# Optimization experiments

Hardware: AMD Instinct MI355X
Metric: run time of the kernel (lower is better)

Reference implementation:

```python
import jax, jax.numpy as jnp
import numpy as np

B, DIM, L, H, W = 4, 128, 256, 8, 8
N = L * H * W
D_INNER, D_STATE, D_CONV, DT_RANK = 128, 8, 4, 8


def _ln(x, w, b, eps=1e-5):
    m = x.mean(-1, keepdims=True)
    v = ((x - m) ** 2).mean(-1, keepdims=True)
    return (x - m) * jax.lax.rsqrt(v + eps) * w + b


def _mamba_fusion(x, z_in, p, i):
    # x, z_in: (B, N, DIM). x drives the SSM; z_in provides the cross-modal gate.
    u = x @ p['Wx'][i]                                    # (B, N, D_INNER)
    z = z_in @ p['Wz'][i]                                 # (B, N, D_INNER)
    # causal depthwise conv1d along tokens, kernel D_CONV (torch pad=k-1 then truncate)
    up = jnp.pad(u, ((0, 0), (D_CONV - 1, 0), (0, 0)))
    w = p['conv_w'][i]                                    # (D_INNER, D_CONV)
    uc = sum(up[:, k:k + u.shape[1], :] * w[:, k] for k in range(D_CONV)) + p['conv_b'][i]
    uc = jax.nn.silu(uc)
    x_dbl = uc @ p['Wxproj'][i]                           # (B, N, DT_RANK + 2*D_STATE)
    dt_r, Bm, Cm = jnp.split(x_dbl, [DT_RANK, DT_RANK + D_STATE], axis=-1)
    dt = jax.nn.softplus(dt_r @ p['Wdt'][i] + p['bdt'][i])  # (B, N, D_INNER)
    A = -jnp.exp(p['A_log'][i])                           # (D_INNER, D_STATE)
    dA = jnp.exp(dt[..., None] * A)                       # (B, N, D_INNER, D_STATE)
    dBu = dt[..., None] * Bm[:, :, None, :] * uc[..., None]

    def step(h, inp):
        dA_t, dBu_t, C_t = inp
        h = dA_t * h + dBu_t                              # (B, D_INNER, D_STATE)
        return h, jnp.einsum('bds,bs->bd', h, C_t)

    h0 = jnp.zeros((u.shape[0], D_INNER, D_STATE), u.dtype)
    _, ys = jax.lax.scan(step, h0, (dA.swapaxes(0, 1), dBu.swapaxes(0, 1), Cm.swapaxes(0, 1)))
    y = ys.swapaxes(0, 1) + p['Dp'][i] * uc
    y = y * jax.nn.silu(z)
    return y @ p['Wout_m'][i] + p['bout_m'][i]


def _cross_block(in0, in1, p, i):
    skip = in0
    a = _ln(in0, p['ln0_w'][i], p['ln0_b'][i])
    b = _ln(in1, p['ln1_w'][i], p['ln1_b'][i])
    return skip + _mamba_fusion(a, b, p, i)


def setup_inputs() -> dict:
    key = jax.random.key(0)
    ks = jax.random.split(key, 16)
    s_in = 1.0 / np.sqrt(DIM)
    s_di = 1.0 / np.sqrt(D_INNER)
    inp = {
        'front': jax.random.normal(ks[0], (B, DIM, L, H, W), jnp.float32),
        'back': jax.random.normal(ks[1], (B, DIM, L, H, W), jnp.float32),
        'ln0_w': jnp.ones((2, DIM), jnp.float32),
        'ln0_b': jnp.zeros((2, DIM), jnp.float32),
        'ln1_w': jnp.ones((2, DIM), jnp.float32),
        'ln1_b': jnp.zeros((2, DIM), jnp.float32),
        'Wx': jax.random.normal(ks[2], (2, DIM, D_INNER), jnp.float32) * s_in,
        'Wz': jax.random.normal(ks[3], (2, DIM, D_INNER), jnp.float32) * s_in,
        'conv_w': jax.random.normal(ks[4], (2, D_INNER, D_CONV), jnp.float32) * 0.5,
        'conv_b': jnp.zeros((2, D_INNER), jnp.float32),
        'Wxproj': jax.random.normal(ks[5], (2, D_INNER, DT_RANK + 2 * D_STATE), jnp.float32) * s_di,
        'Wdt': jax.random.normal(ks[6], (2, DT_RANK, D_INNER), jnp.float32) * (1.0 / np.sqrt(DT_RANK)),
        'bdt': jnp.full((2, D_INNER), -4.6, jnp.float32),  # softplus^-1(~0.01)
        'A_log': jnp.broadcast_to(jnp.log(jnp.arange(1, D_STATE + 1, dtype=jnp.float32)), (2, D_INNER, D_STATE)).copy(),
        'Dp': jnp.ones((2, D_INNER), jnp.float32),
        'Wout_m': jax.random.normal(ks[7], (2, D_INNER, DIM), jnp.float32) * s_di,
        'bout_m': jnp.zeros((2, DIM), jnp.float32),
        'Wout': jax.random.normal(ks[8], (DIM, DIM), jnp.float32) * s_in,
        'bout': jnp.zeros((DIM,), jnp.float32),
    }
    return inp


def reference(front, back, ln0_w, ln0_b, ln1_w, ln1_b, Wx, Wz, conv_w, conv_b,
              Wxproj, Wdt, bdt, A_log, Dp, Wout_m, bout_m, Wout, bout):
    p = dict(ln0_w=ln0_w, ln0_b=ln0_b, ln1_w=ln1_w, ln1_b=ln1_b, Wx=Wx, Wz=Wz,
             conv_w=conv_w, conv_b=conv_b, Wxproj=Wxproj, Wdt=Wdt, bdt=bdt,
             A_log=A_log, Dp=Dp, Wout_m=Wout_m, bout_m=bout_m)
    ff = front.reshape(B, DIM, N).swapaxes(1, 2)          # (B, N, DIM)
    bf = back.reshape(B, DIM, N).swapaxes(1, 2)
    f_fus = _cross_block(ff, bf, p, 0)
    b_fus = _cross_block(bf, ff, p, 1)
    fusion = ((f_fus + b_fus) * 0.5) @ Wout + bout
    return fusion.swapaxes(1, 2).reshape(B, DIM, L, H, W)
```

## Files before the change

kernel.cpp:

```cpp
#include <hip/hip_runtime.h>

#define DEV static __device__ __forceinline__

typedef short s16x8 __attribute__((ext_vector_type(8)));
typedef float f32x4 __attribute__((ext_vector_type(4)));
typedef unsigned short u16;

DEV float b2f(u16 u){ return __uint_as_float(((unsigned int)u) << 16); }
DEV u16 f2b(float f){
  unsigned int x = __float_as_uint(f);
  x += 0x7fffu + ((x >> 16) & 1u);
  return (u16)(x >> 16);
}
DEV float silu_f(float x){ return x * __builtin_amdgcn_rcpf(1.f + __expf(-x)); }
DEV float softplus_f(float x){ return (x > 15.f) ? x : __logf(1.f + __expf(x)); }
DEV bool detf32(const void* lnw){ return *(const unsigned int*)lnw == 0x3F800000u; }
DEV float ldin(const void* p, long long i, bool f){
  return f ? ((const float*)p)[i] : b2f(((const u16*)p)[i]);
}

static constexpr int BATCH = 4;
static constexpr int NSEQ  = 16384;
static constexpr int RTOT  = BATCH * NSEQ;
static constexpr int GCH   = 256;
static constexpr int DIRSZ = BATCH*GCH*128*8;

__global__ __launch_bounds__(256) void k_setup(
                        const void* ln0w, const void* ln0b, const void* ln1w, const void* ln1b,
                        const void* Wx, const void* Wz, const void* Wxp, const void* Wdt,
                        const void* bdt, const void* Alog, const void* convw, const void* convb,
                        const void* Dpr, const void* Woutm, const void* boutm,
                        const void* Wout, const void* bout,
                        u16* Wuz, u16* WdtBC, u16* Wcat, u16* WoutT,
                        float* buz, float* bdtf, float* bcat, float* boutf,
                        float* Aexp, float* convwF, float* convbF, float* DpF)
{
  bool f = detf32(ln0w);
  int tid = blockIdx.x * 256 + threadIdx.x;
  int gs  = gridDim.x * 256;
  for (int idx = tid; idx < 2*256*128; idx += gs){
    int d = idx >> 15; int n = (idx >> 7) & 255; int k = idx & 127;
    float wv;
    if (n < 128) wv = ldin(ln0w, d*128+k, f) * ldin(Wx, (long long)(d*128+k)*128 + n, f);
    else         wv = ldin(ln1w, (1-d)*128+k, f) * ldin(Wz, (long long)((1-d)*128+k)*128 + (n-128), f);
    Wuz[idx] = f2b(wv);
  }
  for (int idx = tid; idx < 2*256; idx += gs){
    int d = idx >> 8; int n = idx & 255;
    float s = 0.f;
    if (n < 128){
      for (int k = 0; k < 128; ++k)
        s += ldin(ln0b, d*128+k, f) * ldin(Wx, (long long)(d*128+k)*128 + n, f);
    } else {
      for (int k = 0; k < 128; ++k)
        s += ldin(ln1b, (1-d)*128+k, f) * ldin(Wz, (long long)((1-d)*128+k)*128 + (n-128), f);
    }
    buz[idx] = s;
  }
  for (int idx = tid; idx < 2*128; idx += gs)
    bdtf[idx] = ldin(bdt, idx, f);
  for (int idx = tid; idx < 2*144*128; idx += gs){
    int i = idx / (144*128); int rem = idx % (144*128); int n = rem >> 7; int k = rem & 127;
    if (n < 128){
      float s = 0.f;
      for (int j = 0; j < 8; ++j)
        s += ldin(Wxp, (long long)(i*128+k)*24 + j, f) * ldin(Wdt, (long long)(i*8+j)*128 + n, f);
      WdtBC[idx] = f2b(s);
    } else {
      WdtBC[idx] = f2b(ldin(Wxp, (long long)(i*128+k)*24 + (n - 120), f));
    }
  }
  for (int idx = tid; idx < 128*256; idx += gs){
    int n = idx >> 8; int k = idx & 255;
    Wcat[idx] = f2b(ldin(Woutm, (long long)k*128 + n, f));
  }
  for (int idx = tid; idx < 128*128; idx += gs){
    int n = idx >> 7, k = idx & 127;
    WoutT[idx] = f2b(ldin(Wout, (long long)k*128 + n, f));
  }
  for (int idx = tid; idx < 128; idx += gs){
    bcat[idx]  = ldin(boutm, idx, f) + ldin(boutm, 128 + idx, f);
    boutf[idx] = ldin(bout, idx, f);
  }
  for (int idx = tid; idx < 2*128*8; idx += gs)
    Aexp[idx] = -expf(ldin(Alog, idx, f));
  for (int idx = tid; idx < 2*128*4; idx += gs)
    convwF[idx] = ldin(convw, idx, f);
  for (int idx = tid; idx < 2*128; idx += gs){
    convbF[idx] = ldin(convb, idx, f);
    DpF[idx]   = ldin(Dpr, idx, f);
  }
}

__global__ __launch_bounds__(256) void k_ln(const void* front, const void* back, const void* ln0w,
                                            u16* xf, u16* xb, u16* sfbh)
{
  bool fF = detf32(ln0w);
  __shared__ u16 Af[64][130];
  __shared__ u16 Ab[64][130];
  __shared__ float Mf[64], Rf[64], Mb[64], Rb[64];
  int tid = threadIdx.x;
  long long r0 = (long long)blockIdx.x * 64;
  int b  = (int)(r0 >> 14);
  int n0 = (int)(r0 & 16383);
  if (fF){
    const float* fp = (const float*)front;
    const float* bp = (const float*)back;
    for (int it = 0; it < 8; ++it){
      int d = it*16 + (tid >> 4);
      int t = (tid & 15) * 4;
      long long gi = ((long long)(b*128 + d))*NSEQ + n0 + t;
      float4 vf = *(const float4*)&fp[gi];
      float4 vb = *(const float4*)&bp[gi];
      Af[t+0][d] = f2b(vf.x); Af[t+1][d] = f2b(vf.y);
      Af[t+2][d] = f2b(vf.z); Af[t+3][d] = f2b(vf.w);
      Ab[t+0][d] = f2b(vb.x); Ab[t+1][d] = f2b(vb.y);
      Ab[t+2][d] = f2b(vb.z); Ab[t+3][d] = f2b(vb.w);
    }
  } else {
    const u16* fp = (const u16*)front;
    const u16* bp = (const u16*)back;
    for (int it = 0; it < 4; ++it){
      int d = it*32 + (tid >> 3);
      int t = (tid & 7) * 8;
      long long gi = ((long long)(b*128 + d))*NSEQ + n0 + t;
      uint4 vf = *(const uint4*)&fp[gi];
      uint4 vb = *(const uint4*)&bp[gi];
      Af[t+0][d] = (u16)vf.x; Af[t+1][d] = (u16)(vf.x>>16);
      Af[t+2][d] = (u16)vf.y; Af[t+3][d] = (u16)(vf.y>>16);
      Af[t+4][d] = (u16)vf.z; Af[t+5][d] = (u16)(vf.z>>16);
      Af[t+6][d] = (u16)vf.w; Af[t+7][d] = (u16)(vf.w>>16);
      Ab[t+0][d] = (u16)vb.x; Ab[t+1][d] = (u16)(vb.x>>16);
      Ab[t+2][d] = (u16)vb.y; Ab[t+3][d] = (u16)(vb.y>>16);
      Ab[t+4][d] = (u16)vb.z; Ab[t+5][d] = (u16)(vb.z>>16);
      Ab[t+6][d] = (u16)vb.w; Ab[t+7][d] = (u16)(vb.w>>16);
    }
  }
  __syncthreads();
  {
    int t = tid >> 2, sub = tid & 3;
    float s = 0.f, ss = 0.f, s2 = 0.f, ss2 = 0.f;
    for (int k = 0; k < 32; ++k){
      float v = b2f(Af[t][sub*32 + k]); s  += v; ss  += v*v;
      float w = b2f(Ab[t][sub*32 + k]); s2 += w; ss2 += w*w;
    }
    for (int m = 1; m < 4; m <<= 1){
      s  += __shfl_xor(s,  m, 64); ss  += __shfl_xor(ss,  m, 64);
      s2 += __shfl_xor(s2, m, 64); ss2 += __shfl_xor(ss2, m, 64);
    }
    if (sub == 0){
      float mf = s  * (1.f/128.f); float vf = ss  * (1.f/128.f) - mf*mf;
      Mf[t] = mf; Rf[t] = rsqrtf(vf + 1e-5f);
      float mb = s2 * (1.f/128.f); float vb = ss2 * (1.f/128.f) - mb*mb;
      Mb[t] = mb; Rb[t] = rsqrtf(vb + 1e-5f);
    }
  }
  __syncthreads();
  for (int it = 0; it < 8; ++it){
    int t = it*8 + (tid >> 5);
    int c = (tid & 31) * 4;
    float mf = Mf[t], rf = Rf[t], mb = Mb[t], rb = Rb[t];
    float f0 = b2f(Af[t][c+0]), f1 = b2f(Af[t][c+1]), f2 = b2f(Af[t][c+2]), f3 = b2f(Af[t][c+3]);
    float g0 = b2f(Ab[t][c+0]), g1 = b2f(Ab[t][c+1]), g2 = b2f(Ab[t][c+2]), g3 = b2f(Ab[t][c+3]);
    ushort4 xo, zo, so;
    xo.x = f2b((f0-mf)*rf); xo.y = f2b((f1-mf)*rf); xo.z = f2b((f2-mf)*rf); xo.w = f2b((f3-mf)*rf);
    zo.x = f2b((g0-mb)*rb); zo.y = f2b((g1-mb)*rb); zo.z = f2b((g2-mb)*rb); zo.w = f2b((g3-mb)*rb);
    so.x = f2b(f0+g0); so.y = f2b(f1+g1); so.z = f2b(f2+g2); so.w = f2b(f3+g3);
    long long o = (r0 + t)*128 + c;
    *(ushort4*)&xf[o] = xo;
    *(ushort4*)&xb[o] = zo;
    *(ushort4*)&sfbh[o] = so;
  }
}

__global__ __launch_bounds__(256) void k_guz(const u16* __restrict__ xf,
                                             const u16* __restrict__ xb,
                                             const u16* __restrict__ Wuz,
                                             const float* __restrict__ buz,
                                             u16* __restrict__ u0, u16* __restrict__ u1,
                                             u16* __restrict__ z0, u16* __restrict__ z1)
{
  int dir = blockIdx.y;
  const u16* A = dir ? xb : xf;
  const u16* Wt = Wuz + dir*256*128;
  const float* bias = buz + dir*256;
  u16* outU = dir ? u1 : u0;
  u16* outZ = dir ? z0 : z1;
  __shared__ u16 Wl[256][72];
  __shared__ u16 Al[64][72];
  int tid = threadIdx.x;
  long long r0 = (long long)blockIdx.x * 64;
  int w = tid >> 6, lane = tid & 63;
  int q = lane >> 4, m = lane & 15;
  f32x4 acc[16];
  #pragma unroll
  for (int ct = 0; ct < 16; ++ct) acc[ct] = (f32x4){0.f,0.f,0.f,0.f};
  for (int kp = 0; kp < 2; ++kp){
    if (kp) __syncthreads();
    for (int ci = tid; ci < 256*8; ci += 256){
      int n = ci >> 3, c8 = ci & 7;
      *(uint4*)&Wl[n][c8*8] = *(const uint4*)&Wt[n*128 + kp*64 + c8*8];
    }
    for (int ci = tid; ci < 64*8; ci += 256){
      int rl = ci >> 3, c8 = ci & 7;
      *(uint4*)&Al[rl][c8*8] = *(const uint4*)&A[(r0 + rl)*128 + kp*64 + c8*8];
    }
    __syncthreads();
    #pragma unroll
    for (int kt = 0; kt < 2; ++kt){
      s16x8 af = *(const s16x8*)&Al[w*16 + m][kt*32 + q*8];
      #pragma unroll
      for (int ct = 0; ct < 16; ++ct){
        s16x8 bf = *(const s16x8*)&Wl[ct*16 + m][kt*32 + q*8];
        acc[ct] = __builtin_amdgcn_mfma_f32_16x16x32_bf16(af, bf, acc[ct], 0, 0, 0);
      }
    }
  }
  #pragma unroll
  for (int ct = 0; ct < 16; ++ct){
    int col = ct*16 + m;
    #pragma unroll
    for (int i = 0; i < 4; ++i){
      long long r = r0 + w*16 + q*4 + i;
      float v = acc[ct][i] + bias[col];
      if (col < 128) outU[r*128 + col] = f2b(v);
      else           outZ[r*128 + (col - 128)] = f2b(silu_f(v));
    }
  }
}

__global__ __launch_bounds__(256, 4) void k_cps(const u16* __restrict__ u0p,
                                             const u16* __restrict__ u1p,
                                             const float* __restrict__ convwF,
                                             const float* __restrict__ convbF,
                                             const u16* __restrict__ WdtBC,
                                             const float* __restrict__ bdtf,
                                             const float* __restrict__ Aexp,
                                             u16* __restrict__ uc0p, u16* __restrict__ uc1p,
                                             u16* __restrict__ yg,
                                             float* __restrict__ BCg,
                                             float* __restrict__ P, float* __restrict__ Q)
{
  __shared__ u16 Al[64][136];
  __shared__ u16 Dl[64][136];
  __shared__ float BCl[64][16];
  int dir = blockIdx.y;
  const u16* u = dir ? u1p : u0p;
  u16* ucb = dir ? uc1p : uc0p;
  const u16* Wt = WdtBC + dir*18432;
  const float* bias = bdtf + dir*128;
  u16* dtb = yg + dir*128;
  float* BC = BCg + (long long)dir*RTOT*16;
  int tid = threadIdx.x;
  long long r0 = (long long)blockIdx.x * 64;
  int b  = (int)(r0 >> 14);
  int n0 = (int)(r0 & 16383);
  {
    int c = tid & 127, h = tid >> 7;
    const float* wp = &convwF[(dir*128 + c)*4];
    float w0 = wp[0], w1 = wp[1], w2 = wp[2], w3 = wp[3];
    float cb = convbF[dir*128 + c];
    int t0 = h*32;
    const u16* up = u + (long long)b*NSEQ*128 + c;
    int nbase = n0 + t0;
    float win0 = (nbase-3 >= 0) ? b2f(up[(long long)(nbase-3)*128]) : 0.f;
    float win1 = (nbase-2 >= 0) ? b2f(up[(long long)(nbase-2)*128]) : 0.f;
    float win2 = (nbase-1 >= 0) ? b2f(up[(long long)(nbase-1)*128]) : 0.f;
    #pragma unroll
    for (int t = 0; t < 32; ++t){
      float cur = b2f(up[(long long)(nbase + t)*128]);
      float a = win0*w0 + win1*w1 + win2*w2 + cur*w3 + cb;
      u16 s = f2b(silu_f(a));
      Al[t0 + t][c] = s;
      ucb[(r0 + t0 + t)*128 + c] = s;
      win0 = win1; win1 = win2; win2 = cur;
    }
  }
  __syncthreads();
  int w = tid >> 6, lane = tid & 63;
  int q = lane >> 4, m = lane & 15;
  f32x4 acc[9];
  #pragma unroll
  for (int ct = 0; ct < 9; ++ct) acc[ct] = (f32x4){0.f,0.f,0.f,0.f};
  #pragma unroll
  for (int kt = 0; kt < 4; ++kt){
    s16x8 af = *(const s16x8*)&Al[w*16 + m][kt*32 + q*8];
    const u16* wrow = Wt + m*128 + kt*32 + q*8;
    #pragma unroll
    for (int ct = 0; ct < 9; ++ct){
      s16x8 bf = *(const s16x8*)&wrow[ct*16*128];
      acc[ct] = __builtin_amdgcn_mfma_f32_16x16x32_bf16(af, bf, acc[ct], 0, 0, 0);
    }
  }
  #pragma unroll
  for (int ct = 0; ct < 9; ++ct){
    int col = ct*16 + m;
    #pragma unroll
    for (int i = 0; i < 4; ++i){
      int rl = w*16 + q*4 + i;
      long long r = r0 + rl;
      float v = acc[ct][i];
      if (col < 128){
        u16 dv = f2b(softplus_f(v + bias[col]));
        dtb[r*256 + col] = dv;
        Dl[rl][col] = dv;
      } else {
        BC[r*16 + (col - 128)] = v;
        BCl[rl][col - 128] = v;
      }
    }
  }
  __syncthreads();
  {
    int c = tid & 127, sh = tid >> 7;
    int g = (int)(r0 & 16383) >> 6;
    int base = sh*4;
    float Ac[4], Pr[4], H[4];
    bool fast = true;
    #pragma unroll
    for (int j = 0; j < 4; ++j){
      Ac[j] = Aexp[(dir*128 + c)*8 + base + j];
      fast = fast && (fabsf(Ac[j] + (float)(base + j + 1)) < 2e-4f);
      Pr[j] = 1.f; H[j] = 0.f;
    }
    if (fast){
      for (int t = 0; t < 64; ++t){
        float d  = b2f(Dl[t][c]);
        float uu = b2f(Al[t][c]);
        float du = d * uu;
        float E  = __expf(-d);
        float E2 = E*E, E3 = E2*E, E4 = E2*E2;
        float M  = base ? E4 : 1.f;
        float dA0 = M*E, dA1 = M*E2, dA2 = M*E3, dA3 = M*E4;
        H[0] = dA0*H[0] + du*BCl[t][base+0]; Pr[0] *= dA0;
        H[1] = dA1*H[1] + du*BCl[t][base+1]; Pr[1] *= dA1;
        H[2] = dA2*H[2] + du*BCl[t][base+2]; Pr[2] *= dA2;
        H[3] = dA3*H[3] + du*BCl[t][base+3]; Pr[3] *= dA3;
      }
    } else {
      for (int t = 0; t < 64; ++t){
        float d  = b2f(Dl[t][c]);
        float uu = b2f(Al[t][c]);
        float du = d * uu;
        #pragma unroll
        for (int j = 0; j < 4; ++j){
          float dA = __expf(d * Ac[j]);
          H[j]  = dA*H[j] + du*BCl[t][base + j];
          Pr[j] *= dA;
        }
      }
    }
    long long o = (long long)dir*DIRSZ + (((long long)b*GCH + g)*128 + c)*8 + base;
    *(float4*)&P[o] = make_float4(Pr[0],Pr[1],Pr[2],Pr[3]);
    *(float4*)&Q[o] = make_float4(H[0],H[1],H[2],H[3]);
  }
}

__global__ __launch_bounds__(64) void k_scan2(const float* __restrict__ P,
                                              const float* __restrict__ Q,
                                              float* __restrict__ hinit)
{
  int idx = blockIdx.x*64 + threadIdx.x;
  int dir = idx >> 12;
  int rem = idx & 4095;
  int b  = rem >> 10;
  int cs = rem & 1023;
  long long base = (long long)dir*DIRSZ + (long long)b*GCH*1024 + cs;
  float h = 0.f;
  for (int g = 0; g < GCH; g += 8){
    long long o = base + (long long)g*1024;
    float p[8], qv[8];
    #pragma unroll
    for (int j = 0; j < 8; ++j){ p[j] = P[o + j*1024]; qv[j] = Q[o + j*1024]; }
    #pragma unroll
    for (int j = 0; j < 8; ++j){
      hinit[o + j*1024] = h;
      h = p[j]*h + qv[j];
    }
  }
}

__global__ __launch_bounds__(256) void k_scan3(const u16* __restrict__ uc0p,
                                               const u16* __restrict__ uc1p,
                                               const float* __restrict__ BCg,
                                               const float* __restrict__ hinit,
                                               const u16* __restrict__ z0p,
                                               const u16* __restrict__ z1p,
                                               const float* __restrict__ DpF,
                                               const float* __restrict__ Aexp,
                                               u16* yg)
{
  __shared__ float Bl[128][8];
  __shared__ float Cl[128][8];
  int dir = blockIdx.y;
  const u16* uc = dir ? uc1p : uc0p;
  const u16* zs = dir ? z1p : z0p;
  const float* BC = BCg + (long long)dir*RTOT*16;
  int tid = threadIdx.x;
  int gp = blockIdx.x & 127;
  int b  = blockIdx.x >> 7;
  long long tokbase = (long long)b*NSEQ + gp*128;
  for (int idx = tid; idx < 128*8; idx += 256){
    int row = idx >> 3, s = idx & 7;
    Bl[row][s] = BC[(tokbase + row)*16 + s];
    Cl[row][s] = BC[(tokbase + row)*16 + 8 + s];
  }
  __syncthreads();
  int c = tid & 127;
  int gh = tid >> 7;
  int g = gp*2 + gh;
  int doff = dir*128;
  float Ac[8], H[8];
  long long ho = (long long)dir*DIRSZ + (((long long)b*GCH + g)*128 + c)*8;
  float4 h0 = *(const float4*)&hinit[ho];
  float4 h1 = *(const float4*)&hinit[ho + 4];
  H[0]=h0.x; H[1]=h0.y; H[2]=h0.z; H[3]=h0.w;
  H[4]=h1.x; H[5]=h1.y; H[6]=h1.z; H[7]=h1.w;
  bool fast = true;
  #pragma unroll
  for (int s = 0; s < 8; ++s){
    Ac[s] = Aexp[(dir*128 + c)*8 + s];
    fast = fast && (fabsf(Ac[s] + (float)(s + 1)) < 2e-4f);
  }
  float dpc = DpF[dir*128 + c];
  long long rbase = (long long)b*NSEQ + g*64;
  if (fast){
    for (int t = 0; t < 64; ++t){
      long long r = rbase + t;
      float d  = b2f(yg[r*256 + doff + c]);
      float uu = b2f(uc[r*128 + c]);
      float du = d * uu;
      int rowl = gh*64 + t;
      float E  = __expf(-d);
      float E2 = E*E, E3 = E2*E, E4 = E2*E2;
      float dA[8] = {E, E2, E3, E4, E4*E, E4*E2, E4*E3, E4*E4};
      float y = 0.f;
      #pragma unroll
      for (int s = 0; s < 8; ++s){
        H[s] = dA[s]*H[s] + du*Bl[rowl][s];
        y += H[s]*Cl[rowl][s];
      }
      float zv = b2f(zs[r*128 + c]);
      yg[r*256 + doff + c] = f2b((y + dpc*uu) * zv);
    }
  } else {
    for (int t = 0; t < 64; ++t){
      long long r = rbase + t;
      float d  = b2f(yg[r*256 + doff + c]);
      float uu = b2f(uc[r*128 + c]);
      float du = d * uu;
      int rowl = gh*64 + t;
      float y = 0.f;
      #pragma unroll
      for (int s = 0; s < 8; ++s){
        float dA = __expf(d * Ac[s]);
        H[s] = dA*H[s] + du*Bl[rowl][s];
        y += H[s]*Cl[rowl][s];
      }
      float zv = b2f(zs[r*128 + c]);
      yg[r*256 + doff + c] = f2b((y + dpc*uu) * zv);
    }
  }
}

__global__ __launch_bounds__(256) void k_tail(const u16* __restrict__ yg,
                                              const u16* __restrict__ Wcat,
                                              const float* __restrict__ bcat,
                                              const u16* __restrict__ sfbh,
                                              const u16* __restrict__ WoutT,
                                              const float* __restrict__ boutf,
                                              void* outp, const void* dflag)
{
  __shared__ u16 Wl[128][136];
  __shared__ u16 Al[64][136];
  __shared__ u16 Sl[64][136];
  int tid = threadIdx.x;
  long long r0 = (long long)blockIdx.x * 64;
  int w = tid >> 6, lane = tid & 63;
  int q = lane >> 4, m = lane & 15;
  f32x4 acc[8];
  #pragma unroll
  for (int ct = 0; ct < 8; ++ct) acc[ct] = (f32x4){0.f,0.f,0.f,0.f};
  for (int kp = 0; kp < 2; ++kp){
    if (kp) __syncthreads();
    for (int ci = tid; ci < 128*16; ci += 256){
      int n = ci >> 4, c8 = ci & 15;
      *(uint4*)&Wl[n][c8*8] = *(const uint4*)&Wcat[n*256 + kp*128 + c8*8];
    }
    for (int ci = tid; ci < 64*16; ci += 256){
      int rl = ci >> 4, c8 = ci & 15;
      *(uint4*)&Al[rl][c8*8] = *(const uint4*)&yg[(r0 + rl)*256 + kp*128 + c8*8];
    }
    __syncthreads();
    #pragma unroll
    for (int kt = 0; kt < 4; ++kt){
      s16x8 af = *(const s16x8*)&Al[w*16 + m][kt*32 + q*8];
      #pragma unroll
      for (int ct = 0; ct < 8; ++ct){
        s16x8 bf = *(const s16x8*)&Wl[ct*16 + m][kt*32 + q*8];
        acc[ct] = __builtin_amdgcn_mfma_f32_16x16x32_bf16(af, bf, acc[ct], 0, 0, 0);
      }
    }
  }
  #pragma unroll
  for (int ct = 0; ct < 8; ++ct){
    int col = ct*16 + m;
    #pragma unroll
    for (int i = 0; i < 4; ++i){
      int rl = w*16 + q*4 + i;
      long long r = r0 + rl;
      Sl[rl][col] = f2b(acc[ct][i] + bcat[col] + b2f(sfbh[r*128 + col]));
    }
  }
  __syncthreads();
  for (int ci = tid; ci < 128*16; ci += 256){
    int n = ci >> 4, c8 = ci & 15;
    *(uint4*)&Wl[n][c8*8] = *(const uint4*)&WoutT[n*128 + c8*8];
  }
  __syncthreads();
  f32x4 acc2[8];
  #pragma unroll
  for (int ct = 0; ct < 8; ++ct) acc2[ct] = (f32x4){0.f,0.f,0.f,0.f};
  #pragma unroll
  for (int kt = 0; kt < 4; ++kt){
    s16x8 af = *(const s16x8*)&Sl[w*16 + m][kt*32 + q*8];
    #pragma unroll
    for (int ct = 0; ct < 8; ++ct){
      s16x8 bf = *(const s16x8*)&Wl[ct*16 + m][kt*32 + q*8];
      acc2[ct] = __builtin_amdgcn_mfma_f32_16x16x32_bf16(af, bf, acc2[ct], 0, 0, 0);
    }
  }
  u16* Tl = &Al[0][0];
  #pragma unroll
  for (int ct = 0; ct < 8; ++ct){
    int col = ct*16 + m;
    #pragma unroll
    for (int i = 0; i < 4; ++i){
      int rl = w*16 + q*4 + i;
      Tl[col*68 + rl] = f2b(0.5f*acc2[ct][i] + boutf[col]);
    }
  }
  __syncthreads();
  long long b = r0 >> 14; long long tok0 = r0 & 16383;
  bool fo = detf32(dflag);
  if (fo){
    float* of = (float*)outp;
    for (int idx = tid; idx < 128*16; idx += 256){
      int n = idx >> 4; int t0 = (idx & 15)*4;
      float4 v;
      v.x = b2f(Tl[n*68 + t0+0]); v.y = b2f(Tl[n*68 + t0+1]);
      v.z = b2f(Tl[n*68 + t0+2]); v.w = b2f(Tl[n*68 + t0+3]);
      *(float4*)&of[(((long long)(b*128 + n)) << 14) + tok0 + t0] = v;
    }
  } else {
    u16* ob = (u16*)outp;
    for (int idx = tid; idx < 128*16; idx += 256){
      int n = idx >> 4; int t0 = (idx & 15)*4;
      ushort4 v;
      v.x = Tl[n*68 + t0+0]; v.y = Tl[n*68 + t0+1];
      v.z = Tl[n*68 + t0+2]; v.w = Tl[n*68 + t0+3];
      *(ushort4*)&ob[(((long long)(b*128 + n)) << 14) + tok0 + t0] = v;
    }
  }
}

extern "C" void kernel_launch(void* const* d_in, const int* in_sizes, int n_in,
                              void* d_out, int out_size, void* d_ws, size_t ws_size,
                              hipStream_t stream)
{
  (void)in_sizes; (void)n_in; (void)out_size; (void)ws_size;
  const void* front = d_in[0];
  const void* back  = d_in[1];
  const void* ln0w  = d_in[2];
  const void* ln0b  = d_in[3];
  const void* ln1w  = d_in[4];
  const void* ln1b  = d_in[5];
  const void* Wx    = d_in[6];
  const void* Wz    = d_in[7];
  const void* convw = d_in[8];
  const void* convb = d_in[9];
  const void* Wxp   = d_in[10];
  const void* Wdt   = d_in[11];
  const void* bdt   = d_in[12];
  const void* Alog  = d_in[13];
  const void* Dpr   = d_in[14];
  const void* Woutm = d_in[15];
  const void* boutm = d_in[16];
  const void* Wout  = d_in[17];
  const void* bout  = d_in[18];

  char* p = (char*)d_ws;
  auto alloc = [&](size_t bytes) -> void* {
    void* q = (void*)p; p += (bytes + 255) & ~(size_t)255; return q;
  };
  u16*   xf    = (u16*)  alloc((size_t)RTOT*128*2);
  u16*   xb    = (u16*)  alloc((size_t)RTOT*128*2);
  u16*   sfbh  = (u16*)  alloc((size_t)RTOT*128*2);
  u16*   u0    = (u16*)  alloc((size_t)RTOT*128*2);
  u16*   u1    = (u16*)  alloc((size_t)RTOT*128*2);
  u16*   z0    = (u16*)  alloc((size_t)RTOT*128*2);
  u16*   z1    = (u16*)  alloc((size_t)RTOT*128*2);
  float* BC    = (float*)alloc((size_t)2*RTOT*16*4);
  float* Pb    = (float*)alloc((size_t)2*DIRSZ*4);
  float* Qb    = (float*)alloc((size_t)2*DIRSZ*4);
  float* hin   = (float*)alloc((size_t)2*DIRSZ*4);
  u16*   yg    = (u16*)  alloc((size_t)RTOT*256*2);
  u16*   Wuz   = (u16*)  alloc(2*256*128*2);
  u16*   WdtBC = (u16*)  alloc(2*144*128*2);
  u16*   Wcat  = (u16*)  alloc(128*256*2);
  u16*   WoutT = (u16*)  alloc(128*128*2);
  float* buz   = (float*)alloc(2*256*4);
  float* bdtf  = (float*)alloc(2*128*4);
  float* bcat  = (float*)alloc(128*4);
  float* boutf = (float*)alloc(128*4);
  float* Aexp  = (float*)alloc(2*128*8*4);
  float* convwF= (float*)alloc(2*128*4*4);
  float* convbF= (float*)alloc(2*128*4);
  float* DpF   = (float*)alloc(2*128*4);

  k_setup<<<128,256,0,stream>>>(ln0w,ln0b,ln1w,ln1b,Wx,Wz,Wxp,Wdt,bdt,Alog,convw,convb,Dpr,
                                Woutm,boutm,Wout,bout,
                                Wuz,WdtBC,Wcat,WoutT,buz,bdtf,bcat,boutf,Aexp,
                                convwF,convbF,DpF);
  k_ln<<<RTOT/64,256,0,stream>>>(front,back,ln0w,xf,xb,sfbh);

  dim3 g2(RTOT/64, 2);
  k_guz<<<g2,256,0,stream>>>(xf, xb, Wuz, buz, u0, u1, z0, z1);
  k_cps<<<g2,256,0,stream>>>(u0, u1, convwF, convbF, WdtBC, bdtf, Aexp,
                             xf, xb, yg, BC, Pb, Qb);
  k_scan2<<<128,64,0,stream>>>(Pb, Qb, hin);
  dim3 g3(BATCH*GCH/2, 2);
  k_scan3<<<g3,256,0,stream>>>(xf, xb, BC, hin, z0, z1, DpF, Aexp, yg);
  k_tail<<<RTOT/64,256,0,stream>>>(yg, Wcat, bcat, sfbh, WoutT, boutf, d_out, ln0w);
}
```

Before: 339.7 us.

## Stage dt/BC projection weights in XOR-swizzled LDS inside k_cps

k_cps now copies the 144x128 bf16 projection weight tile into shared memory once per block instead of each wave reading it from global memory for the MFMA B operand. The activation tile uses an XOR swizzle in place of row padding to avoid bank conflicts. The weight buffer is then reused for the dt and BC tiles after a barrier. LDS use per block rises, so the occupancy hint drops from 4 to 3 blocks per CU, and the extra barrier plus weight staging add per-block latency.

```diff
diff --git a/kernel.cpp b/kernel.cpp
--- a/kernel.cpp
+++ b/kernel.cpp
@@ -24,6 +24,8 @@
 static constexpr int RTOT  = BATCH * NSEQ;
 static constexpr int GCH   = 256;
 static constexpr int DIRSZ = BATCH*GCH*128*8;
+
+DEV int swz(int row, int col){ return (row << 7) + (col ^ ((row & 7) << 3)); }
 
 __global__ __launch_bounds__(256) void k_setup(
                         const void* ln0w, const void* ln0b, const void* ln1w, const void* ln1b,
@@ -229,7 +231,7 @@
   }
 }
 
-__global__ __launch_bounds__(256, 4) void k_cps(const u16* __restrict__ u0p,
+__global__ __launch_bounds__(256, 3) void k_cps(const u16* __restrict__ u0p,
                                              const u16* __restrict__ u1p,
                                              const float* __restrict__ convwF,
                                              const float* __restrict__ convbF,
@@ -241,9 +243,8 @@
                                              float* __restrict__ BCg,
                                              float* __restrict__ P, float* __restrict__ Q)
 {
-  __shared__ u16 Al[64][136];
-  __shared__ u16 Dl[64][136];
-  __shared__ float BCl[64][16];
+  __shared__ __align__(16) u16 AlF[64*128];
+  __shared__ __align__(16) u16 WlF[144*128];
   int dir = blockIdx.y;
   const u16* u = dir ? u1p : u0p;
   u16* ucb = dir ? uc1p : uc0p;
@@ -255,6 +256,10 @@
   long long r0 = (long long)blockIdx.x * 64;
   int b  = (int)(r0 >> 14);
   int n0 = (int)(r0 & 16383);
+  for (int ci = tid; ci < 144*16; ci += 256){
+    int n = ci >> 4, c8 = ci & 15;
+    *(uint4*)&WlF[(n << 7) + ((c8 ^ (n & 7)) << 3)] = *(const uint4*)&Wt[n*128 + c8*8];
+  }
   {
     int c = tid & 127, h = tid >> 7;
     const float* wp = &convwF[(dir*128 + c)*4];
@@ -271,7 +276,7 @@
       float cur = b2f(up[(long long)(nbase + t)*128]);
       float a = win0*w0 + win1*w1 + win2*w2 + cur*w3 + cb;
       u16 s = f2b(silu_f(a));
-      Al[t0 + t][c] = s;
+      AlF[swz(t0 + t, c)] = s;
       ucb[(r0 + t0 + t)*128 + c] = s;
       win0 = win1; win1 = win2; win2 = cur;
     }
@@ -284,14 +289,17 @@
   for (int ct = 0; ct < 9; ++ct) acc[ct] = (f32x4){0.f,0.f,0.f,0.f};
   #pragma unroll
   for (int kt = 0; kt < 4; ++kt){
-    s16x8 af = *(const s16x8*)&Al[w*16 + m][kt*32 + q*8];
-    const u16* wrow = Wt + m*128 + kt*32 + q*8;
+    int sc = (kt*32 + q*8) ^ ((m & 7) << 3);
+    s16x8 af = *(const s16x8*)&AlF[((w*16 + m) << 7) + sc];
     #pragma unroll
     for (int ct = 0; ct < 9; ++ct){
-      s16x8 bf = *(const s16x8*)&wrow[ct*16*128];
+      s16x8 bf = *(const s16x8*)&WlF[((ct*16 + m) << 7) + sc];
       acc[ct] = __builtin_amdgcn_mfma_f32_16x16x32_bf16(af, bf, acc[ct], 0, 0, 0);
     }
   }
+  __syncthreads();
+  u16* Dl = WlF;
+  float* BCl = (float*)&WlF[64*128];
   #pragma unroll
   for (int ct = 0; ct < 9; ++ct){
     int col = ct*16 + m;
@@ -303,10 +311,10 @@
       if (col < 128){
         u16 dv = f2b(softplus_f(v + bias[col]));
         dtb[r*256 + col] = dv;
-        Dl[rl][col] = dv;
+        Dl[swz(rl, col)] = dv;
       } else {
         BC[r*16 + (col - 128)] = v;
-        BCl[rl][col - 128] = v;
+        BCl[rl*16 + (col - 128)] = v;
       }
     }
   }
@@ -325,27 +333,29 @@
     }
     if (fast){
       for (int t = 0; t < 64; ++t){
-        float d  = b2f(Dl[t][c]);
-        float uu = b2f(Al[t][c]);
+        int ce = swz(t, c);
+        float d  = b2f(Dl[ce]);
+        float uu = b2f(AlF[ce]);
         float du = d * uu;
         float E  = __expf(-d);
         float E2 = E*E, E3 = E2*E, E4 = E2*E2;
         float M  = base ? E4 : 1.f;
         float dA0 = M*E, dA1 = M*E2, dA2 = M*E3, dA3 = M*E4;
-        H[0] = dA0*H[0] + du*BCl[t][base+0]; Pr[0] *= dA0;
-        H[1] = dA1*H[1] + du*BCl[t][base+1]; Pr[1] *= dA1;
-        H[2] = dA2*H[2] + du*BCl[t][base+2]; Pr[2] *= dA2;
-        H[3] = dA3*H[3] + du*BCl[t][base+3]; Pr[3] *= dA3;
+        H[0] = dA0*H[0] + du*BCl[t*16 + base+0]; Pr[0] *= dA0;
+        H[1] = dA1*H[1] + du*BCl[t*16 + base+1]; Pr[1] *= dA1;
+        H[2] = dA2*H[2] + du*BCl[t*16 + base+2]; Pr[2] *= dA2;
+        H[3] = dA3*H[3] + du*BCl[t*16 + base+3]; Pr[3] *= dA3;
       }
     } else {
       for (int t = 0; t < 64; ++t){
-        float d  = b2f(Dl[t][c]);
-        float uu = b2f(Al[t][c]);
+        int ce = swz(t, c);
+        float d  = b2f(Dl[ce]);
+        float uu = b2f(AlF[ce]);
         float du = d * uu;
         #pragma unroll
         for (int j = 0; j < 4; ++j){
           float dA = __expf(d * Ac[j]);
-          H[j]  = dA*H[j] + du*BCl[t][base + j];
+          H[j]  = dA*H[j] + du*BCl[t*16 + base + j];
           Pr[j] *= dA;
         }
       }
```

New measurement: 329.4 us. 1.03x faster.
